# Kernel optimization log

Hardware: AMD Instinct MI355X
Metric: run time of the kernel (lower is better)

Reference implementation:

```python
import jax, jax.numpy as jnp
import numpy as np

B, D_IN, H, D_OUT, E = 16384, 512, 1024, 512, 4


def setup_inputs() -> dict:
    key = jax.random.key(0)
    ks = jax.random.split(key, 8)
    x = jax.random.normal(ks[0], (B, D_IN), dtype=jnp.float32)
    command = jax.random.randint(ks[1], (B,), 0, E, dtype=jnp.int64)
    # Per-branch Encoder params: Linear(D_IN->H), Linear(H->H), Linear(H->D_OUT)
    s = 0.02
    W1 = jax.random.normal(ks[2], (E, D_IN, H), dtype=jnp.float32) * s
    b1 = jnp.zeros((E, H), dtype=jnp.float32)
    W2 = jax.random.normal(ks[3], (E, H, H), dtype=jnp.float32) * s
    b2 = jnp.zeros((E, H), dtype=jnp.float32)
    W3 = jax.random.normal(ks[4], (E, H, D_OUT), dtype=jnp.float32) * s
    b3 = jnp.zeros((E, D_OUT), dtype=jnp.float32)
    return {"x": x, "command": command, "W1": W1, "b1": b1,
            "W2": W2, "b2": b2, "W3": W3, "b3": b3}


def reference(x, command, W1, b1, W2, b2, W3, b3):
    # Evaluate all branches as batched GEMMs, then select per-sample branch.
    # Mathematically identical to per-sample dispatch in the torch module.
    h = jax.nn.relu(jnp.einsum('bi,eih->beh', x, W1) + b1)        # [B,E,H]
    h = jax.nn.relu(jnp.einsum('beh,ehk->bek', h, W2) + b2)       # [B,E,H]
    y = jnp.tanh(jnp.einsum('bek,eko->beo', h, W3) + b3)          # [B,E,D_OUT]
    # select branch output per sample according to command
    idx = command.astype(jnp.int32)[:, None, None]                # [B,1,1]
    out = jnp.take_along_axis(y, idx, axis=1)[:, 0, :]            # [B,D_OUT]
    return out
```

## Files before the change

### kernel.cpp

```cpp
#include <hip/hip_runtime.h>


#define B_N   16384
#define DIN   512
#define HID   1024
#define DOUT  512
#define MAXTILES 136

typedef __attribute__((ext_vector_type(8))) short bf16x8;
typedef __attribute__((ext_vector_type(4))) float f32x4;
typedef __attribute__((address_space(3))) unsigned int lds_u32;
typedef const __attribute__((address_space(1))) unsigned int glb_u32;

__device__ __forceinline__ void gll16(const void* g, void* l) {
    __builtin_amdgcn_global_load_lds((glb_u32*)g, (lds_u32*)l, 16, 0, 0);
}

__device__ __forceinline__ unsigned short f2bf(float f) {
    unsigned int u = __float_as_uint(f);
    u += 0x7FFFu + ((u >> 16) & 1u);
    return (unsigned short)(u >> 16);
}

__device__ __forceinline__ float fast_tanh(float x) {
    x = fminf(fmaxf(x, -9.0f), 9.0f);
    float t = __builtin_amdgcn_exp2f(x * 2.8853900817779268f);
    return (t - 1.0f) * __builtin_amdgcn_rcpf(t + 1.0f);
}

__global__ void plan_all_k(const int* __restrict__ cmd, int* __restrict__ ctrl,
                           int* __restrict__ tileExpert, int* __restrict__ tileBase) {
    __shared__ int h[4];
    int tid = threadIdx.x;
    if (tid < 4) h[tid] = 0;
    __syncthreads();
    int c0 = 0, c1 = 0, c2 = 0, c3 = 0;
    for (int i = tid; i < B_N; i += 256) {
        int e = cmd[i] & 3;
        c0 += (e == 0); c1 += (e == 1); c2 += (e == 2); c3 += (e == 3);
    }
    atomicAdd(&h[0], c0); atomicAdd(&h[1], c1);
    atomicAdd(&h[2], c2); atomicAdd(&h[3], c3);
    __syncthreads();
    if (tid == 0) {
        int P = 0, nt = 0;
        for (int e = 0; e < 4; ++e) {
            ctrl[e] = h[e];
            ctrl[4 + e] = 0;
            ctrl[8 + e] = P;
            int tiles = (h[e] + 127) >> 7;
            for (int t = 0; t < tiles; ++t) {
                tileExpert[nt] = e;
                tileBase[nt] = P + t * 128;
                ++nt;
            }
            P += tiles * 128;
        }
        ctrl[12] = P;
        ctrl[13] = nt;
    }
}

__global__ void scatter_k(const int* __restrict__ cmd, int* __restrict__ ctrl,
                          int* __restrict__ perm) {
    int i = blockIdx.x * 256 + threadIdx.x;
    int e = cmd[i] & 3;
    int lane = threadIdx.x & 63;
#pragma unroll
    for (int ee = 0; ee < 4; ++ee) {
        unsigned long long mask = __ballot(e == ee);
        if (e == ee) {
            int leader = __ffsll((unsigned long long)mask) - 1;
            int rank = __popcll(mask & ((1ull << lane) - 1ull));
            int wbase = 0;
            if (lane == leader)
                wbase = atomicAdd(&ctrl[4 + ee], __popcll(mask));
            wbase = __builtin_amdgcn_readfirstlane(wbase);
            perm[ctrl[8 + ee] + wbase + rank] = i;
        }
    }
}

__global__ __launch_bounds__(256) void prep_data_k(
    const float* __restrict__ W1, const float* __restrict__ W2,
    const float* __restrict__ W3, unsigned short* __restrict__ Wt1,
    unsigned short* __restrict__ Wt2, unsigned short* __restrict__ Wt3,
    const float* __restrict__ x, unsigned short* __restrict__ xp,
    int* __restrict__ perm, const int* __restrict__ ctrl)
{
    int b = blockIdx.x;
    if (b < 8192) {
        int e = b >> 11, r = b & 2047;
        const float* W; unsigned short* Wt; int KD, ND, kt, nt;
        if (r < 512)       { W = W1; Wt = Wt1; KD = 512;  ND = 1024; kt = r & 15;           nt = r >> 4; }
        else if (r < 1536) { W = W2; Wt = Wt2; KD = 1024; ND = 1024; kt = (r - 512) & 31;   nt = (r - 512) >> 5; }
        else               { W = W3; Wt = Wt3; KD = 1024; ND = 512;  kt = (r - 1536) & 31;  nt = (r - 1536) >> 5; }
        __shared__ float t[32][33];
        size_t base = (size_t)e * KD * ND;
        int k0 = kt * 32, n0 = nt * 32;
        int tx = threadIdx.x & 31, ty = threadIdx.x >> 5;
#pragma unroll
        for (int s = 0; s < 4; ++s)
            t[ty + s * 8][tx] = W[base + (size_t)(k0 + ty + s * 8) * ND + n0 + tx];
        __syncthreads();
#pragma unroll
        for (int s = 0; s < 4; ++s)
            Wt[base + (size_t)(n0 + ty + s * 8) * KD + k0 + tx] = f2bf(t[tx][ty + s * 8]);
    } else {
        int g = b - 8192;
        int p = g * 4 + (int)(threadIdx.x >> 6);
        if (p >= ctrl[12]) return;
        int lane = threadIdx.x & 63;
        int e = (p >= ctrl[9]) + (p >= ctrl[10]) + (p >= ctrl[11]);
        int segBase = ctrl[8 + e];
        int src;
        if (p < segBase + ctrl[e]) {
            src = perm[p];
        } else {
            src = perm[segBase];
            if (lane == 0) perm[p] = src;
        }
        const float* xr = x + (size_t)src * DIN + lane * 8;
        float4 a = *(const float4*)xr;
        float4 c = *(const float4*)(xr + 4);
        uint4 o;
        o.x = (unsigned)f2bf(a.x) | ((unsigned)f2bf(a.y) << 16);
        o.y = (unsigned)f2bf(a.z) | ((unsigned)f2bf(a.w) << 16);
        o.z = (unsigned)f2bf(c.x) | ((unsigned)f2bf(c.y) << 16);
        o.w = (unsigned)f2bf(c.z) | ((unsigned)f2bf(c.w) << 16);
        *(uint4*)(xp + (size_t)p * DIN + lane * 8) = o;
    }
}

template<int K, int N, int ACT, bool SCATTER_OUT>
__global__ __launch_bounds__(256) void gemm_k(
    const unsigned short* __restrict__ A, const unsigned short* __restrict__ Bt,
    const float* __restrict__ bias, void* __restrict__ Outp,
    const int* __restrict__ ctrl, const int* __restrict__ tileExpert,
    const int* __restrict__ tileBase, const int* __restrict__ perm)
{
    if ((int)blockIdx.x >= ctrl[13]) return;
    const int e = tileExpert[blockIdx.x];
    const int rowBase = tileBase[blockIdx.x];
    const int n0 = blockIdx.y * 128;

    __shared__ unsigned short Als[128 * 64];
    __shared__ unsigned short Bls[128 * 64];

    const int tid = threadIdx.x;
    const int lane = tid & 63;
    const int w = tid >> 6;
    const int wm = w >> 1, wn = w & 1;
    const int lr = lane & 15, lh = lane >> 4;

    f32x4 acc[4][4] = {};

    const int tr = tid >> 3;
    const int tc = tid & 7;
    const int cs = (tc ^ (tr & 7)) * 8;
    const unsigned short* As = A + (size_t)(rowBase + tr) * K + cs;
    const unsigned short* Bs = Bt + ((size_t)e * N + n0 + tr) * K + cs;
    const int ldst = tr * 64 + tc * 8;

    constexpr int NK = K / 64;
    for (int kq = 0; kq < NK; ++kq) {
        const int k0 = kq * 64;
        __syncthreads();
#pragma unroll
        for (int j = 0; j < 4; ++j) {
            gll16(As + (size_t)(j * 32) * K + k0, &Als[j * 2048 + ldst]);
            gll16(Bs + (size_t)(j * 32) * K + k0, &Bls[j * 2048 + ldst]);
        }
        __syncthreads();
#pragma unroll
        for (int kk = 0; kk < 2; ++kk) {
            const int ksl = ((kk * 4 + lh) ^ (lr & 7)) * 8;
            bf16x8 afr[4], bfr[4];
#pragma unroll
            for (int mi = 0; mi < 4; ++mi)
                afr[mi] = *(const bf16x8*)&Als[(wm * 64 + mi * 16 + lr) * 64 + ksl];
#pragma unroll
            for (int ni = 0; ni < 4; ++ni)
                bfr[ni] = *(const bf16x8*)&Bls[(wn * 64 + ni * 16 + lr) * 64 + ksl];
#pragma unroll
            for (int mi = 0; mi < 4; ++mi)
#pragma unroll
                for (int ni = 0; ni < 4; ++ni)
                    acc[mi][ni] = __builtin_amdgcn_mfma_f32_16x16x32_bf16(
                        afr[mi], bfr[ni], acc[mi][ni], 0, 0, 0);
        }
    }

    float bv[4];
    int colv[4];
#pragma unroll
    for (int ni = 0; ni < 4; ++ni) {
        colv[ni] = n0 + wn * 64 + ni * 16 + lr;
        bv[ni] = bias[e * N + colv[ni]];
    }
#pragma unroll
    for (int mi = 0; mi < 4; ++mi) {
#pragma unroll
        for (int r = 0; r < 4; ++r) {
            int rowL = wm * 64 + mi * 16 + lh * 4 + r;
            int gRow = rowBase + rowL;
            int orow = SCATTER_OUT ? perm[gRow] : gRow;
#pragma unroll
            for (int ni = 0; ni < 4; ++ni) {
                float v = acc[mi][ni][r] + bv[ni];
                if (ACT == 0) v = fmaxf(v, 0.0f);
                else          v = fast_tanh(v);
                if (SCATTER_OUT)
                    ((float*)Outp)[(size_t)orow * N + colv[ni]] = v;
                else
                    ((unsigned short*)Outp)[(size_t)orow * N + colv[ni]] = f2bf(v);
            }
        }
    }
}

extern "C" void kernel_launch(void* const* d_in, const int* in_sizes, int n_in,
                              void* d_out, int out_size, void* d_ws, size_t ws_size,
                              hipStream_t stream) {
    const float* x  = (const float*)d_in[0];
    const int*   cmd= (const int*)d_in[1];
    const float* W1 = (const float*)d_in[2];
    const float* b1 = (const float*)d_in[3];
    const float* W2 = (const float*)d_in[4];
    const float* b2 = (const float*)d_in[5];
    const float* W3 = (const float*)d_in[6];
    const float* b3 = (const float*)d_in[7];
    float* out = (float*)d_out;

    char* w = (char*)d_ws;
    int* ctrl       = (int*)w;
    int* tileExpert = ctrl + 64;
    int* tileBase   = ctrl + 224;
    int* perm       = ctrl + 512;
    unsigned short* Wt1 = (unsigned short*)(w + 131072);
    unsigned short* Wt2 = (unsigned short*)(w + 131072 + 4194304);
    unsigned short* Wt3 = (unsigned short*)(w + 131072 + 12582912);
    unsigned short* h1  = (unsigned short*)(w + 131072 + 16777216);
    unsigned short* h2  = h1 + (size_t)16896 * HID;
    unsigned short* xp  = h2;

    plan_all_k<<<1, 256, 0, stream>>>(cmd, ctrl, tileExpert, tileBase);
    scatter_k<<<B_N / 256, 256, 0, stream>>>(cmd, ctrl, perm);
    prep_data_k<<<8192 + 4224, 256, 0, stream>>>(W1, W2, W3, Wt1, Wt2, Wt3,
                                                 x, xp, perm, ctrl);

    gemm_k<DIN, HID, 0, false><<<dim3(MAXTILES, 8), 256, 0, stream>>>(
        xp, Wt1, b1, h1, ctrl, tileExpert, tileBase, perm);
    gemm_k<HID, HID, 0, false><<<dim3(MAXTILES, 8), 256, 0, stream>>>(
        h1, Wt2, b2, h2, ctrl, tileExpert, tileBase, perm);
    gemm_k<HID, DOUT, 1, true><<<dim3(MAXTILES, 4), 256, 0, stream>>>(
        h2, Wt3, b3, out, ctrl, tileExpert, tileBase, perm);
}
```

Baseline: 167.9 us.

## Swizzle GEMM block-to-tile mapping across XCDs and pack transposed weight stores

Each GEMM block's linear id is remapped so that blocks sharing a row tile and its N panels spread round-robin over the 8 XCD groups (l&7), keeping all panels of one row tile on the same chiplet so A-tile reuse hits its L2. The weight transpose epilogue now writes two packed bf16 values per 32-bit store instead of single 16-bit stores, which halves the store instruction count. The swizzle assumes MAXTILES*PN equals 8*17*PN and that the hardware dispatches blocks round-robin to XCDs.

```diff
diff --git a/kernel.cpp b/kernel.cpp
--- a/kernel.cpp
+++ b/kernel.cpp
@@ -103,9 +103,14 @@
         for (int s = 0; s < 4; ++s)
             t[ty + s * 8][tx] = W[base + (size_t)(k0 + ty + s * 8) * ND + n0 + tx];
         __syncthreads();
-#pragma unroll
-        for (int s = 0; s < 4; ++s)
-            Wt[base + (size_t)(n0 + ty + s * 8) * KD + k0 + tx] = f2bf(t[tx][ty + s * 8]);
+        int tx2 = (threadIdx.x & 15) * 2, ny = threadIdx.x >> 4;
+#pragma unroll
+        for (int s = 0; s < 2; ++s) {
+            int n = ny + s * 16;
+            unsigned int v = (unsigned)f2bf(t[tx2][n])
+                           | ((unsigned)f2bf(t[tx2 + 1][n]) << 16);
+            *(unsigned int*)&Wt[base + (size_t)(n0 + n) * KD + k0 + tx2] = v;
+        }
     } else {
         int g = b - 8192;
         int p = g * 4 + (int)(threadIdx.x >> 6);
@@ -132,17 +137,22 @@
     }
 }
 
-template<int K, int N, int ACT, bool SCATTER_OUT>
+template<int K, int N, int PN, int ACT, bool SCATTER_OUT>
 __global__ __launch_bounds__(256) void gemm_k(
     const unsigned short* __restrict__ A, const unsigned short* __restrict__ Bt,
     const float* __restrict__ bias, void* __restrict__ Outp,
     const int* __restrict__ ctrl, const int* __restrict__ tileExpert,
     const int* __restrict__ tileBase, const int* __restrict__ perm)
 {
-    if ((int)blockIdx.x >= ctrl[13]) return;
-    const int e = tileExpert[blockIdx.x];
-    const int rowBase = tileBase[blockIdx.x];
-    const int n0 = blockIdx.y * 128;
+    static_assert(PN == 4 || PN == 8, "PN power of 2");
+    const int l = (int)blockIdx.x + MAXTILES * (int)blockIdx.y;
+    const int swz = (l & 7) * (17 * PN) + (l >> 3);
+    const int tile = swz / PN;
+    const int panel = swz & (PN - 1);
+    if (tile >= ctrl[13]) return;
+    const int e = tileExpert[tile];
+    const int rowBase = tileBase[tile];
+    const int n0 = panel * 128;
 
     __shared__ unsigned short Als[128 * 64];
     __shared__ unsigned short Bls[128 * 64];
@@ -249,10 +259,10 @@
     prep_data_k<<<8192 + 4224, 256, 0, stream>>>(W1, W2, W3, Wt1, Wt2, Wt3,
                                                  x, xp, perm, ctrl);
 
-    gemm_k<DIN, HID, 0, false><<<dim3(MAXTILES, 8), 256, 0, stream>>>(
+    gemm_k<DIN, HID, 8, 0, false><<<dim3(MAXTILES, 8), 256, 0, stream>>>(
         xp, Wt1, b1, h1, ctrl, tileExpert, tileBase, perm);
-    gemm_k<HID, HID, 0, false><<<dim3(MAXTILES, 8), 256, 0, stream>>>(
+    gemm_k<HID, HID, 8, 0, false><<<dim3(MAXTILES, 8), 256, 0, stream>>>(
         h1, Wt2, b2, h2, ctrl, tileExpert, tileBase, perm);
-    gemm_k<HID, DOUT, 1, true><<<dim3(MAXTILES, 4), 256, 0, stream>>>(
+    gemm_k<HID, DOUT, 4, 1, true><<<dim3(MAXTILES, 4), 256, 0, stream>>>(
         h2, Wt3, b3, out, ctrl, tileExpert, tileBase, perm);
 }
```

Result: faster. 163.8 us (-2.5%).
